# Kernel tuning notes

Hardware: AMD Instinct MI355X
Metric: run time of the kernel (lower is better)

Reference implementation:

```python
import jax, jax.numpy as jnp
import numpy as np

B, N, F_IN, HID, OUT, NHEADS = 16, 1024, 64, 64, 64, 4
TAXI = 512        # get_Parameter('taxi_size') from the original repo (node split point)
ALPHA = 0.2       # LeakyReLU negative slope


def setup_inputs() -> dict:
    key = jax.random.key(0)
    ks = jax.random.split(key, 8)
    x = jax.random.normal(ks[0], (B, N, F_IN), dtype=jnp.float32)
    # multiplicative binary mask (mostly ones so softmax rows are well-conditioned)
    mask = (jax.random.uniform(ks[1], (N, N)) > 0.1).astype(jnp.float32)
    s_in = 1.0 / np.sqrt(F_IN)
    s_cat = 1.0 / np.sqrt(NHEADS * HID)
    W1 = jax.random.normal(ks[2], (NHEADS, F_IN, HID), jnp.float32) * s_in
    W2 = jax.random.normal(ks[3], (NHEADS, F_IN, HID), jnp.float32) * s_in
    a = jax.random.normal(ks[4], (NHEADS, 2 * HID), jnp.float32) * 0.1
    W1o = jax.random.normal(ks[5], (NHEADS * HID, OUT), jnp.float32) * s_cat
    W2o = jax.random.normal(ks[6], (NHEADS * HID, OUT), jnp.float32) * s_cat
    ao = jax.random.normal(ks[7], (2 * OUT,), jnp.float32) * 0.1
    return dict(x=x, mask=mask, W1=W1, W2=W2, a=a, W1o=W1o, W2o=W2o, ao=ao)


def _gat_layer(x, mask, W1, W2, a, out_dim):
    # x: [B,N,F]; W1,W2: [F,out_dim]; a: [2*out_dim]
    # node-group-split linear projection (taxi nodes via W1, rest via W2)
    h = jnp.concatenate([x[:, :TAXI] @ W1, x[:, TAXI:] @ W2], axis=1)  # [B,N,O]
    A1 = h @ a[:out_dim]                 # [B,N]
    A2 = h @ a[out_dim:]                 # [B,N]
    sim = A1[:, :, None] + A2[:, None, :]  # [B,N,N] additive scores
    e = jax.nn.leaky_relu(sim, ALPHA)
    e = mask[None, :, :] * e             # multiplicative mask (as in source)
    attn = jax.nn.softmax(e, axis=-1)    # [B,N,N]  (dropout omitted: eval mode)
    h_prime = jnp.einsum('bnm,bmo->bno', attn, h)
    return jax.nn.elu(h_prime), attn


def reference(x, mask, W1, W2, a, W1o, W2o, ao):
    # input dropout omitted (eval mode)
    heads = [_gat_layer(x, mask, W1[i], W2[i], a[i], HID)[0] for i in range(NHEADS)]
    xc = jnp.concatenate(heads, axis=-1)          # [B,N,NHEADS*HID]
    out, attn = _gat_layer(xc, mask, W1o, W2o, ao, OUT)
    return out, attn
```

## Files before the change

### kernel.cpp

```cpp
#include <hip/hip_runtime.h>
#include <hip/hip_bf16.h>

#define B_      16
#define N_      1024
#define ALPHA_  0.2f
#define LOG2E_  1.4426950408889634f

typedef __attribute__((ext_vector_type(8)))  __bf16 bf16x8;
typedef __attribute__((ext_vector_type(4)))  float  floatx4;
typedef __attribute__((ext_vector_type(16))) float  floatx16;

__device__ __forceinline__ float eluf(float u) { return u > 0.f ? u : __expf(u) - 1.f; }

__device__ __forceinline__ float exp2fast(float x) {
#if __has_builtin(__builtin_amdgcn_exp2f)
    return __builtin_amdgcn_exp2f(x);
#else
    return exp2f(x);
#endif
}

__device__ __forceinline__ floatx4 mfma_bf16(bf16x8 a, bf16x8 b, floatx4 c) {
    return __builtin_amdgcn_mfma_f32_16x16x32_bf16(a, b, c, 0, 0, 0);
}
__device__ __forceinline__ floatx16 mfma32_bf16(bf16x8 a, bf16x8 b, floatx16 c) {
    return __builtin_amdgcn_mfma_f32_32x32x16_bf16(a, b, c, 0, 0, 0);
}

__global__ __launch_bounds__(256) void proj1_kernel(
    const float* __restrict__ x, const float* __restrict__ W1,
    const float* __restrict__ W2, const float* __restrict__ av,
    const float* __restrict__ maskG, unsigned* __restrict__ bitsOut,
    __bf16* __restrict__ h1t, float* __restrict__ A1, float* __restrict__ A2)
{
    const int tile = blockIdx.x, b = blockIdx.y, head = blockIdx.z;
    const int n0 = tile * 64;
    const float* W  = ((n0 < 512) ? W1 : W2) + head * 64 * 64;
    const float* ah = av + head * 128;

    __shared__ __align__(16) __bf16 xs[64][72];
    __shared__ __align__(16) __bf16 Wt[64][72];
    __shared__ __align__(16) float as_[128];

    const int tid = threadIdx.x;
    if (tid < 128) as_[tid] = ah[tid];
#pragma unroll
    for (int i = 0; i < 4; ++i) {
        int idx = i * 256 + tid;
        int r = idx >> 4, c = (idx & 15) * 4;
        float4 v = *(const float4*)(x + ((size_t)(b * N_ + n0 + r)) * 64 + c);
        xs[r][c+0] = (__bf16)v.x; xs[r][c+1] = (__bf16)v.y;
        xs[r][c+2] = (__bf16)v.z; xs[r][c+3] = (__bf16)v.w;
        float4 wv = *(const float4*)(W + (size_t)r * 64 + c);
        Wt[c+0][r] = (__bf16)wv.x; Wt[c+1][r] = (__bf16)wv.y;
        Wt[c+2][r] = (__bf16)wv.z; Wt[c+3][r] = (__bf16)wv.w;
    }

    {
        const int bid = blockIdx.x + 16 * (blockIdx.y + 16 * blockIdx.z);
        if (tid < 32) {
            const float* src = maskG + ((size_t)(bid * 32 + tid)) * 32;
            unsigned v = 0;
#pragma unroll
            for (int j = 0; j < 8; ++j) {
                float4 f = *(const float4*)(src + j * 4);
                v |= ((unsigned)(f.x != 0.f)) << (j * 4 + 0);
                v |= ((unsigned)(f.y != 0.f)) << (j * 4 + 1);
                v |= ((unsigned)(f.z != 0.f)) << (j * 4 + 2);
                v |= ((unsigned)(f.w != 0.f)) << (j * 4 + 3);
            }
            bitsOut[bid * 32 + tid] = v;
        }
    }
    __syncthreads();

    const int w = tid >> 6, L = tid & 63, quad = L >> 4, lo = L & 15;
    floatx4 acc[4] = {{0,0,0,0},{0,0,0,0},{0,0,0,0},{0,0,0,0}};
#pragma unroll
    for (int kc = 0; kc < 2; ++kc) {
        bf16x8 af = *(bf16x8*)&xs[16 * w + lo][kc * 32 + quad * 8];
#pragma unroll
        for (int t = 0; t < 4; ++t) {
            bf16x8 bv = *(bf16x8*)&Wt[16 * t + lo][kc * 32 + quad * 8];
            acc[t] = mfma_bf16(af, bv, acc[t]);
        }
    }

    float p1[4] = {0, 0, 0, 0}, p2[4] = {0, 0, 0, 0};
#pragma unroll
    for (int t = 0; t < 4; ++t) {
        float a1w = as_[16 * t + lo], a2w = as_[64 + 16 * t + lo];
#pragma unroll
        for (int i = 0; i < 4; ++i) { p1[i] += acc[t][i] * a1w; p2[i] += acc[t][i] * a2w; }
    }
#pragma unroll
    for (int s = 1; s < 16; s <<= 1)
#pragma unroll
        for (int i = 0; i < 4; ++i) {
            p1[i] += __shfl_xor(p1[i], s);
            p2[i] += __shfl_xor(p2[i], s);
        }
    const int bh = head * B_ + b;
    if (lo == 0) {
#pragma unroll
        for (int i = 0; i < 4; ++i) {
            int n = 16 * w + quad * 4 + i;
            A1[bh * N_ + n0 + n] = p1[i] * LOG2E_;
            A2[bh * N_ + n0 + n] = p2[i] * LOG2E_;
        }
    }

    __syncthreads();
#pragma unroll
    for (int t = 0; t < 4; ++t)
#pragma unroll
        for (int i = 0; i < 4; ++i)
            xs[16 * w + quad * 4 + i][16 * t + lo] = (__bf16)acc[t][i];
    __syncthreads();
    const int d = tid & 63, ch = tid >> 6;
    bf16x8 v0, v1;
#pragma unroll
    for (int j = 0; j < 8; ++j) v0[j] = xs[ch * 16 + j][d];
#pragma unroll
    for (int j = 0; j < 8; ++j) v1[j] = xs[ch * 16 + 8 + j][d];
    bf16x8* dst = (bf16x8*)(h1t + ((size_t)bh * 64 + d) * N_ + n0 + ch * 16);
    dst[0] = v0; dst[1] = v1;
}

__global__ __launch_bounds__(256) void attn1_kernel(
    const float* __restrict__ A1g, const float* __restrict__ A2g,
    const __bf16* __restrict__ Htg, const unsigned* __restrict__ bitsG,
    __bf16* __restrict__ xc_out)
{
    const int b = blockIdx.x, head = blockIdx.y, tile = blockIdx.z;
    const int n0 = tile * 128;
    const int bh = head * B_ + b;
    const float* A2 = A2g + (size_t)bh * N_;
    const __bf16* Hglob = Htg + (size_t)bh * 64 * N_;

    __shared__ __align__(16) __bf16 frag[2][4][2][64][8];
    __shared__ __align__(16) __bf16 ts[128][72];
    __shared__ __align__(16) float A2s[N_];
    __shared__ __align__(16) unsigned bitsS[32 * 128];
    __shared__ float invzS[128];

    const int tid = threadIdx.x;
    *(float4*)&A2s[tid * 4] = *(const float4*)(A2 + tid * 4);
    {
        const int row = tid >> 1, w0 = (tid & 1) * 16;
        uint4 u0 = *(const uint4*)(bitsG + n0 * 32 + tid * 16);
        uint4 u1 = *(const uint4*)(bitsG + n0 * 32 + tid * 16 + 4);
        uint4 u2 = *(const uint4*)(bitsG + n0 * 32 + tid * 16 + 8);
        uint4 u3 = *(const uint4*)(bitsG + n0 * 32 + tid * 16 + 12);
        bitsS[(w0+ 0)*128+row] = u0.x; bitsS[(w0+ 1)*128+row] = u0.y;
        bitsS[(w0+ 2)*128+row] = u0.z; bitsS[(w0+ 3)*128+row] = u0.w;
        bitsS[(w0+ 4)*128+row] = u1.x; bitsS[(w0+ 5)*128+row] = u1.y;
        bitsS[(w0+ 6)*128+row] = u1.z; bitsS[(w0+ 7)*128+row] = u1.w;
        bitsS[(w0+ 8)*128+row] = u2.x; bitsS[(w0+ 9)*128+row] = u2.y;
        bitsS[(w0+10)*128+row] = u2.z; bitsS[(w0+11)*128+row] = u2.w;
        bitsS[(w0+12)*128+row] = u3.x; bitsS[(w0+13)*128+row] = u3.y;
        bitsS[(w0+14)*128+row] = u3.z; bitsS[(w0+15)*128+row] = u3.w;
    }

    const int sd = tid >> 2, sq = tid & 3;
    const __bf16* hrow = Hglob + (size_t)sd * N_ + sq * 16;
    const int L = tid & 63, rg = tid >> 6, hi = L >> 5, lq = L & 31;
    const int rloc = rg * 32 + lq;
    const float a1r = A1g[(size_t)bh * N_ + n0 + rloc];

    bf16x8 h0 = *(const bf16x8*)(hrow);
    bf16x8 h1 = *(const bf16x8*)(hrow + 8);
    *(bf16x8*)&frag[0][sq][sd >> 5][(sd & 31)][0]      = h0;
    *(bf16x8*)&frag[0][sq][sd >> 5][(sd & 31) + 32][0] = h1;
    __syncthreads();

    floatx16 acc0 = {0,0,0,0,0,0,0,0,0,0,0,0,0,0,0,0};
    floatx16 acc1 = {0,0,0,0,0,0,0,0,0,0,0,0,0,0,0,0};
    float zacc = 0.f;

    for (int mt = 0; mt < 16; ++mt) {
        const int cur = mt & 1;
        if (mt < 15) {
            h0 = *(const bf16x8*)(hrow + (mt + 1) * 64);
            h1 = *(const bf16x8*)(hrow + (mt + 1) * 64 + 8);
        }
#pragma unroll
        for (int ks = 0; ks < 4; ++ks) {
            const int mbase = mt * 64 + ks * 16 + hi * 8;
            const unsigned wb = bitsS[(mbase >> 5) * 128 + rloc] >> (mbase & 31);
            float4 av  = *(const float4*)&A2s[mbase];
            float4 av2 = *(const float4*)&A2s[mbase + 4];
            float a2v[8] = {av.x, av.y, av.z, av.w, av2.x, av2.y, av2.z, av2.w};
            float o[8];
#pragma unroll
            for (int j = 0; j < 8; ++j) {
                float s = a1r + a2v[j];
                float lr = fmaxf(s, ALPHA_ * s);
                int bm = (int)(wb << (31 - j)) >> 31;
                lr = __int_as_float(__float_as_int(lr) & bm);
                float t = exp2fast(lr);
                zacc += t; o[j] = t;
            }
            bf16x8 af = {(__bf16)o[0], (__bf16)o[1], (__bf16)o[2], (__bf16)o[3],
                         (__bf16)o[4], (__bf16)o[5], (__bf16)o[6], (__bf16)o[7]};
            bf16x8 bv0 = *(bf16x8*)&frag[cur][ks][0][L][0];
            bf16x8 bv1 = *(bf16x8*)&frag[cur][ks][1][L][0];
            acc0 = mfma32_bf16(af, bv0, acc0);
            acc1 = mfma32_bf16(af, bv1, acc1);
        }
        if (mt < 15) {
            *(bf16x8*)&frag[cur ^ 1][sq][sd >> 5][(sd & 31)][0]      = h0;
            *(bf16x8*)&frag[cur ^ 1][sq][sd >> 5][(sd & 31) + 32][0] = h1;
            __syncthreads();
        }
    }

    zacc += __shfl_xor(zacc, 32);
    if (hi == 0) invzS[rloc] = 1.f / zacc;
    __syncthreads();

    float iz[16];
#pragma unroll
    for (int r = 0; r < 16; ++r)
        iz[r] = invzS[rg * 32 + (r & 3) + 8 * (r >> 2) + 4 * hi];

#pragma unroll
    for (int r = 0; r < 16; ++r) {
        const int row = rg * 32 + (r & 3) + 8 * (r >> 2) + 4 * hi;
        ts[row][lq]      = (__bf16)eluf(acc0[r] * iz[r]);
        ts[row][32 + lq] = (__bf16)eluf(acc1[r] * iz[r]);
    }
    __syncthreads();
#pragma unroll
    for (int i = 0; i < 4; ++i) {
        int cid = i * 256 + tid;
        int row = cid >> 3, c8 = (cid & 7) * 8;
        bf16x8 v = *(bf16x8*)&ts[row][c8];
        *(bf16x8*)(xc_out + ((size_t)(b * N_ + n0 + row)) * 256 + head * 64 + c8) = v;
    }
}

__global__ __launch_bounds__(256) void attn2_kernel(
    const float* __restrict__ A1g, const float* __restrict__ A2g,
    const __bf16* __restrict__ Htg, const unsigned* __restrict__ bitsG,
    float* __restrict__ out_f, float* __restrict__ attn_f)
{
    const int b = blockIdx.x, tile = blockIdx.z;
    const int n0 = tile * 32;
    const float* A2 = A2g + (size_t)b * N_;
    const __bf16* Hglob = Htg + (size_t)b * 64 * N_;

    __shared__ __align__(16) __bf16 ts2[2][32][72];
    __shared__ __align__(16) __bf16 Ht2[2][64][72];
    __shared__ __align__(16) float A2s[N_];
    __shared__ __align__(16) unsigned bitsS[1024];
    __shared__ float invz[32];

    const int tid = threadIdx.x;
    *(float4*)&A2s[tid * 4] = *(const float4*)(A2 + tid * 4);
    {
        uint4 u = *(const uint4*)(bitsG + n0 * 32 + tid * 4);
        const int row = tid >> 3, wb0 = (tid & 7) * 4;
        bitsS[(wb0+0)*32+row] = u.x; bitsS[(wb0+1)*32+row] = u.y;
        bitsS[(wb0+2)*32+row] = u.z; bitsS[(wb0+3)*32+row] = u.w;
    }

    const int r2 = tid >> 3, q2 = tid & 7;
    const float a1r = A1g[(size_t)b * N_ + n0 + r2];
    const int dr = tid >> 2, dq = tid & 3;
    const int w = tid >> 6, L = tid & 63, quad = L >> 4, lo = L & 15;
    const __bf16* hrow = Hglob + (size_t)dr * N_ + dq * 16;

    floatx4 acc2[2] = {{0,0,0,0},{0,0,0,0}};
    float zacc = 0.f;
    bf16x8 tr[16];

    __syncthreads();

    auto scores = [&](int mt) -> bf16x8 {
        const int mb = mt * 64 + q2 * 8;
        const unsigned wb = bitsS[(mt * 2 + (q2 >> 2)) * 32 + r2] >> ((q2 & 3) * 8);
        float4 alo = *(const float4*)&A2s[mb];
        float4 ahi = *(const float4*)&A2s[mb + 4];
        float a2v[8] = {alo.x, alo.y, alo.z, alo.w, ahi.x, ahi.y, ahi.z, ahi.w};
        float o[8];
#pragma unroll
        for (int j = 0; j < 8; ++j) {
            float s = a1r + a2v[j];
            float lr = fmaxf(s, ALPHA_ * s);
            int bm = (int)(wb << (31 - j)) >> 31;
            lr = __int_as_float(__float_as_int(lr) & bm);
            float t = exp2fast(lr);
            zacc += t; o[j] = t;
        }
        bf16x8 pk = {(__bf16)o[0], (__bf16)o[1], (__bf16)o[2], (__bf16)o[3],
                     (__bf16)o[4], (__bf16)o[5], (__bf16)o[6], (__bf16)o[7]};
        return pk;
    };

    {
        bf16x8 h0 = *(const bf16x8*)(hrow);
        bf16x8 h1 = *(const bf16x8*)(hrow + 8);
        bf16x8 pk = scores(0);
        tr[0] = pk;
        *(bf16x8*)&ts2[0][r2][q2 * 8]      = pk;
        *(bf16x8*)&Ht2[0][dr][dq * 16]     = h0;
        *(bf16x8*)&Ht2[0][dr][dq * 16 + 8] = h1;
    }
    __syncthreads();

#pragma unroll
    for (int mt = 0; mt < 16; ++mt) {
        const int cur = mt & 1;
        bf16x8 h0, h1, pk;
        if (mt < 15) {
            h0 = *(const bf16x8*)(hrow + (mt + 1) * 64);
            h1 = *(const bf16x8*)(hrow + (mt + 1) * 64 + 8);
            pk = scores(mt + 1);
            tr[mt + 1] = pk;
        }
#pragma unroll
        for (int c = 0; c < 2; ++c)
#pragma unroll
            for (int rt = 0; rt < 2; ++rt) {
                bf16x8 af = *(bf16x8*)&ts2[cur][16 * rt + lo][c * 32 + quad * 8];
                bf16x8 bv = *(bf16x8*)&Ht2[cur][16 * w + lo][c * 32 + quad * 8];
                acc2[rt] = mfma_bf16(af, bv, acc2[rt]);
            }
        if (mt < 15) {
            *(bf16x8*)&ts2[cur ^ 1][r2][q2 * 8]      = pk;
            *(bf16x8*)&Ht2[cur ^ 1][dr][dq * 16]     = h0;
            *(bf16x8*)&Ht2[cur ^ 1][dr][dq * 16 + 8] = h1;
            __syncthreads();
        }
    }

    zacc += __shfl_xor(zacc, 1);
    zacc += __shfl_xor(zacc, 2);
    zacc += __shfl_xor(zacc, 4);
    if (q2 == 0) invz[r2] = 1.f / zacc;
    __syncthreads();

#pragma unroll
    for (int rt = 0; rt < 2; ++rt)
#pragma unroll
        for (int i = 0; i < 4; ++i) {
            const int n = 16 * rt + quad * 4 + i;
            out_f[((size_t)(b * N_ + n0 + n)) * 64 + 16 * w + lo] =
                eluf(acc2[rt][i] * invz[n]);
        }

    const float iz = invz[r2];
    float* arow = attn_f + ((size_t)(b * N_ + n0 + r2)) * N_ + q2 * 8;
#pragma unroll
    for (int mt = 0; mt < 16; ++mt) {
        bf16x8 t8 = tr[mt];
        float4 f0 = make_float4((float)t8[0] * iz, (float)t8[1] * iz,
                                (float)t8[2] * iz, (float)t8[3] * iz);
        float4 f1 = make_float4((float)t8[4] * iz, (float)t8[5] * iz,
                                (float)t8[6] * iz, (float)t8[7] * iz);
        *(float4*)(arow + mt * 64)     = f0;
        *(float4*)(arow + mt * 64 + 4) = f1;
    }
}

__global__ __launch_bounds__(256) void proj2_kernel(
    const __bf16* __restrict__ xcb, const float* __restrict__ W1o,
    const float* __restrict__ W2o, const float* __restrict__ ao,
    __bf16* __restrict__ h2t, float* __restrict__ A1o, float* __restrict__ A2o)
{
    const int tile = blockIdx.x, b = blockIdx.y;
    const int n0 = tile * 64;
    const float* W = (n0 < 512) ? W1o : W2o;

    __shared__ __align__(16) __bf16 xs[64][264];
    __shared__ __align__(16) __bf16 Wt[64][264];
    __shared__ __align__(16) float as_[128];

    const int tid = threadIdx.x;
    if (tid < 128) as_[tid] = ao[tid];

#pragma unroll
    for (int i = 0; i < 8; ++i) {
        int idx = i * 256 + tid;
        int row = idx >> 5, c = (idx & 31) * 8;
        *(bf16x8*)&xs[row][c] =
            *(const bf16x8*)(xcb + ((size_t)(b * N_ + n0 + row)) * 256 + c);
    }
#pragma unroll
    for (int i = 0; i < 16; ++i) {
        int idx = i * 256 + tid;
        int k = idx >> 4, n4 = (idx & 15) * 4;
        float4 wv = *(const float4*)(W + (size_t)k * 64 + n4);
        Wt[n4 + 0][k] = (__bf16)wv.x;
        Wt[n4 + 1][k] = (__bf16)wv.y;
        Wt[n4 + 2][k] = (__bf16)wv.z;
        Wt[n4 + 3][k] = (__bf16)wv.w;
    }
    __syncthreads();

    const int w = tid >> 6, L = tid & 63, quad = L >> 4, lo = L & 15;
    floatx4 acc[4] = {{0,0,0,0},{0,0,0,0},{0,0,0,0},{0,0,0,0}};
#pragma unroll
    for (int kc = 0; kc < 8; ++kc) {
        bf16x8 af = *(bf16x8*)&xs[16 * w + lo][kc * 32 + quad * 8];
#pragma unroll
        for (int t = 0; t < 4; ++t) {
            bf16x8 bv = *(bf16x8*)&Wt[16 * t + lo][kc * 32 + quad * 8];
            acc[t] = mfma_bf16(af, bv, acc[t]);
        }
    }

    float p1[4] = {0, 0, 0, 0}, p2[4] = {0, 0, 0, 0};
#pragma unroll
    for (int t = 0; t < 4; ++t) {
        float a1w = as_[16 * t + lo], a2w = as_[64 + 16 * t + lo];
#pragma unroll
        for (int i = 0; i < 4; ++i) { p1[i] += acc[t][i] * a1w; p2[i] += acc[t][i] * a2w; }
    }
#pragma unroll
    for (int s = 1; s < 16; s <<= 1)
#pragma unroll
        for (int i = 0; i < 4; ++i) {
            p1[i] += __shfl_xor(p1[i], s);
            p2[i] += __shfl_xor(p2[i], s);
        }
    if (lo == 0) {
#pragma unroll
        for (int i = 0; i < 4; ++i) {
            int n = 16 * w + quad * 4 + i;
            A1o[b * N_ + n0 + n] = p1[i] * LOG2E_;
            A2o[b * N_ + n0 + n] = p2[i] * LOG2E_;
        }
    }

    __syncthreads();
#pragma unroll
    for (int t = 0; t < 4; ++t)
#pragma unroll
        for (int i = 0; i < 4; ++i)
            xs[16 * w + quad * 4 + i][16 * t + lo] = (__bf16)acc[t][i];
    __syncthreads();
    const int d = tid & 63, ch = tid >> 6;
    bf16x8 v0, v1;
#pragma unroll
    for (int j = 0; j < 8; ++j) v0[j] = xs[ch * 16 + j][d];
#pragma unroll
    for (int j = 0; j < 8; ++j) v1[j] = xs[ch * 16 + 8 + j][d];
    bf16x8* dst = (bf16x8*)(h2t + ((size_t)b * 64 + d) * N_ + n0 + ch * 16);
    dst[0] = v0; dst[1] = v1;
}

extern "C" void kernel_launch(void* const* d_in, const int* in_sizes, int n_in,
                              void* d_out, int out_size, void* d_ws, size_t ws_size,
                              hipStream_t stream)
{
    const float* x    = (const float*)d_in[0];
    const float* mask = (const float*)d_in[1];
    const float* W1   = (const float*)d_in[2];
    const float* W2   = (const float*)d_in[3];
    const float* a    = (const float*)d_in[4];
    const float* W1o  = (const float*)d_in[5];
    const float* W2o  = (const float*)d_in[6];
    const float* ao   = (const float*)d_in[7];

    float* out      = (float*)d_out;
    float* attn_out = out + (size_t)B_ * N_ * 64;

    float*    ws    = (float*)d_ws;
    float*    A1    = ws;
    float*    A2    = A1 + 65536;
    float*    A1o   = A2 + 65536;
    float*    A2o   = A1o + 16384;
    __bf16*   h1t   = (__bf16*)(A2o + 16384);
    __bf16*   h2t   = h1t + 4194304;
    __bf16*   xcb   = h2t + 1048576;
    unsigned* bitsG = (unsigned*)(xcb + 4194304);

    proj1_kernel<<<dim3(16, 16, 4), 256, 0, stream>>>(x, W1, W2, a, mask, bitsG,
                                                      h1t, A1, A2);
    attn1_kernel<<<dim3(16, 4, 8), 256, 0, stream>>>(A1, A2, h1t, bitsG, xcb);
    proj2_kernel<<<dim3(16, 16, 1), 256, 0, stream>>>(xcb, W1o, W2o, ao, h2t, A1o, A2o);
    attn2_kernel<<<dim3(16, 1, 32), 256, 0, stream>>>(A1o, A2o, h2t, bitsG, out, attn_out);
}
```

Measured before the change: 150.0 us.

## Merge heads into one proj1 block and alias attn1 shared buffers

proj1 now processes all four heads in one block, with one wave per head. The x tile is loaded once instead of four times, and the grid shrinks from 1024 to 256 blocks. Each wave now does 16 MFMAs per k-chunk, and mask bit packing is redistributed to 128 threads per block. attn1 aliases its frag and ts shared buffers into one pool and adds a launch bound of 4 blocks per CU to raise occupancy, which risks register spills.

```diff
diff --git a/kernel.cpp b/kernel.cpp
--- a/kernel.cpp
+++ b/kernel.cpp
@@ -33,17 +33,17 @@
     const float* __restrict__ maskG, unsigned* __restrict__ bitsOut,
     __bf16* __restrict__ h1t, float* __restrict__ A1, float* __restrict__ A2)
 {
-    const int tile = blockIdx.x, b = blockIdx.y, head = blockIdx.z;
+    const int tile = blockIdx.x, b = blockIdx.y;
     const int n0 = tile * 64;
-    const float* W  = ((n0 < 512) ? W1 : W2) + head * 64 * 64;
-    const float* ah = av + head * 128;
+    const float* Wbase = (n0 < 512) ? W1 : W2;
 
     __shared__ __align__(16) __bf16 xs[64][72];
-    __shared__ __align__(16) __bf16 Wt[64][72];
-    __shared__ __align__(16) float as_[128];
+    __shared__ __align__(16) __bf16 Wth[4][64][72];
+    __shared__ __align__(16) float as_[512];
 
     const int tid = threadIdx.x;
-    if (tid < 128) as_[tid] = ah[tid];
+    *(float2*)&as_[tid * 2] = *(const float2*)(av + tid * 2);
+
 #pragma unroll
     for (int i = 0; i < 4; ++i) {
         int idx = i * 256 + tid;
@@ -51,15 +51,21 @@
         float4 v = *(const float4*)(x + ((size_t)(b * N_ + n0 + r)) * 64 + c);
         xs[r][c+0] = (__bf16)v.x; xs[r][c+1] = (__bf16)v.y;
         xs[r][c+2] = (__bf16)v.z; xs[r][c+3] = (__bf16)v.w;
-        float4 wv = *(const float4*)(W + (size_t)r * 64 + c);
-        Wt[c+0][r] = (__bf16)wv.x; Wt[c+1][r] = (__bf16)wv.y;
-        Wt[c+2][r] = (__bf16)wv.z; Wt[c+3][r] = (__bf16)wv.w;
+    }
+#pragma unroll
+    for (int i = 0; i < 16; ++i) {
+        int idx = i * 256 + tid;
+        int hd = idx >> 10, e = idx & 1023;
+        int r = e >> 4, c = (e & 15) * 4;
+        float4 wv = *(const float4*)(Wbase + hd * 4096 + (size_t)r * 64 + c);
+        Wth[hd][c+0][r] = (__bf16)wv.x; Wth[hd][c+1][r] = (__bf16)wv.y;
+        Wth[hd][c+2][r] = (__bf16)wv.z; Wth[hd][c+3][r] = (__bf16)wv.w;
     }
 
     {
-        const int bid = blockIdx.x + 16 * (blockIdx.y + 16 * blockIdx.z);
-        if (tid < 32) {
-            const float* src = maskG + ((size_t)(bid * 32 + tid)) * 32;
+        const int bid = blockIdx.x + 16 * blockIdx.y;
+        if (tid < 128) {
+            const float* src = maskG + ((size_t)(bid * 128 + tid)) * 32;
             unsigned v = 0;
 #pragma unroll
             for (int j = 0; j < 8; ++j) {
@@ -69,65 +75,80 @@
                 v |= ((unsigned)(f.z != 0.f)) << (j * 4 + 2);
                 v |= ((unsigned)(f.w != 0.f)) << (j * 4 + 3);
             }
-            bitsOut[bid * 32 + tid] = v;
+            bitsOut[bid * 128 + tid] = v;
         }
     }
     __syncthreads();
 
     const int w = tid >> 6, L = tid & 63, quad = L >> 4, lo = L & 15;
-    floatx4 acc[4] = {{0,0,0,0},{0,0,0,0},{0,0,0,0},{0,0,0,0}};
-#pragma unroll
-    for (int kc = 0; kc < 2; ++kc) {
-        bf16x8 af = *(bf16x8*)&xs[16 * w + lo][kc * 32 + quad * 8];
+    floatx4 acc[4][4];
+#pragma unroll
+    for (int m = 0; m < 4; ++m)
+#pragma unroll
+        for (int t = 0; t < 4; ++t) acc[m][t] = floatx4{0, 0, 0, 0};
+
+#pragma unroll
+    for (int kc = 0; kc < 2; ++kc)
+#pragma unroll
+        for (int m = 0; m < 4; ++m) {
+            bf16x8 af = *(bf16x8*)&xs[16 * m + lo][kc * 32 + quad * 8];
+#pragma unroll
+            for (int t = 0; t < 4; ++t) {
+                bf16x8 bv = *(bf16x8*)&Wth[w][16 * t + lo][kc * 32 + quad * 8];
+                acc[m][t] = mfma_bf16(af, bv, acc[m][t]);
+            }
+        }
+
+    const int bh = w * B_ + b;
+#pragma unroll
+    for (int m = 0; m < 4; ++m) {
+        float p1[4] = {0, 0, 0, 0}, p2[4] = {0, 0, 0, 0};
 #pragma unroll
         for (int t = 0; t < 4; ++t) {
-            bf16x8 bv = *(bf16x8*)&Wt[16 * t + lo][kc * 32 + quad * 8];
-            acc[t] = mfma_bf16(af, bv, acc[t]);
-        }
-    }
-
-    float p1[4] = {0, 0, 0, 0}, p2[4] = {0, 0, 0, 0};
-#pragma unroll
-    for (int t = 0; t < 4; ++t) {
-        float a1w = as_[16 * t + lo], a2w = as_[64 + 16 * t + lo];
-#pragma unroll
-        for (int i = 0; i < 4; ++i) { p1[i] += acc[t][i] * a1w; p2[i] += acc[t][i] * a2w; }
-    }
-#pragma unroll
-    for (int s = 1; s < 16; s <<= 1)
-#pragma unroll
-        for (int i = 0; i < 4; ++i) {
-            p1[i] += __shfl_xor(p1[i], s);
-            p2[i] += __shfl_xor(p2[i], s);
-        }
-    const int bh = head * B_ + b;
-    if (lo == 0) {
-#pragma unroll
-        for (int i = 0; i < 4; ++i) {
-            int n = 16 * w + quad * 4 + i;
-            A1[bh * N_ + n0 + n] = p1[i] * LOG2E_;
-            A2[bh * N_ + n0 + n] = p2[i] * LOG2E_;
-        }
-    }
-
-    __syncthreads();
-#pragma unroll
-    for (int t = 0; t < 4; ++t)
-#pragma unroll
-        for (int i = 0; i < 4; ++i)
-            xs[16 * w + quad * 4 + i][16 * t + lo] = (__bf16)acc[t][i];
-    __syncthreads();
-    const int d = tid & 63, ch = tid >> 6;
-    bf16x8 v0, v1;
-#pragma unroll
-    for (int j = 0; j < 8; ++j) v0[j] = xs[ch * 16 + j][d];
-#pragma unroll
-    for (int j = 0; j < 8; ++j) v1[j] = xs[ch * 16 + 8 + j][d];
-    bf16x8* dst = (bf16x8*)(h1t + ((size_t)bh * 64 + d) * N_ + n0 + ch * 16);
-    dst[0] = v0; dst[1] = v1;
-}
-
-__global__ __launch_bounds__(256) void attn1_kernel(
+            float a1w = as_[w * 128 + 16 * t + lo], a2w = as_[w * 128 + 64 + 16 * t + lo];
+#pragma unroll
+            for (int i = 0; i < 4; ++i) { p1[i] += acc[m][t][i] * a1w; p2[i] += acc[m][t][i] * a2w; }
+        }
+#pragma unroll
+        for (int s = 1; s < 16; s <<= 1)
+#pragma unroll
+            for (int i = 0; i < 4; ++i) {
+                p1[i] += __shfl_xor(p1[i], s);
+                p2[i] += __shfl_xor(p2[i], s);
+            }
+        if (lo == 0) {
+#pragma unroll
+            for (int i = 0; i < 4; ++i) {
+                int n = 16 * m + quad * 4 + i;
+                A1[bh * N_ + n0 + n] = p1[i] * LOG2E_;
+                A2[bh * N_ + n0 + n] = p2[i] * LOG2E_;
+            }
+        }
+    }
+
+    __syncthreads();
+#pragma unroll
+    for (int m = 0; m < 4; ++m)
+#pragma unroll
+        for (int t = 0; t < 4; ++t)
+#pragma unroll
+            for (int i = 0; i < 4; ++i)
+                Wth[w][16 * m + quad * 4 + i][16 * t + lo] = (__bf16)acc[m][t][i];
+    __syncthreads();
+    const int d = L;
+#pragma unroll
+    for (int ch = 0; ch < 4; ++ch) {
+        bf16x8 v0, v1;
+#pragma unroll
+        for (int j = 0; j < 8; ++j) v0[j] = Wth[w][ch * 16 + j][d];
+#pragma unroll
+        for (int j = 0; j < 8; ++j) v1[j] = Wth[w][ch * 16 + 8 + j][d];
+        bf16x8* dst = (bf16x8*)(h1t + ((size_t)bh * 64 + d) * N_ + n0 + ch * 16);
+        dst[0] = v0; dst[1] = v1;
+    }
+}
+
+__global__ __launch_bounds__(256, 4) void attn1_kernel(
     const float* __restrict__ A1g, const float* __restrict__ A2g,
     const __bf16* __restrict__ Htg, const unsigned* __restrict__ bitsG,
     __bf16* __restrict__ xc_out)
@@ -138,8 +159,9 @@
     const float* A2 = A2g + (size_t)bh * N_;
     const __bf16* Hglob = Htg + (size_t)bh * 64 * N_;
 
-    __shared__ __align__(16) __bf16 frag[2][4][2][64][8];
-    __shared__ __align__(16) __bf16 ts[128][72];
+    __shared__ __align__(16) char poolc[128 * 72 * 2];
+    __bf16 (*frag)[4][2][64][8] = (__bf16(*)[4][2][64][8])poolc;
+    __bf16 (*ts)[72]            = (__bf16(*)[72])poolc;
     __shared__ __align__(16) float A2s[N_];
     __shared__ __align__(16) unsigned bitsS[32 * 128];
     __shared__ float invzS[128];
@@ -477,8 +499,8 @@
     __bf16*   xcb   = h2t + 1048576;
     unsigned* bitsG = (unsigned*)(xcb + 4194304);
 
-    proj1_kernel<<<dim3(16, 16, 4), 256, 0, stream>>>(x, W1, W2, a, mask, bitsG,
-                                                      h1t, A1, A2);
+    proj1_kernel<<<dim3(16, 16), 256, 0, stream>>>(x, W1, W2, a, mask, bitsG,
+                                                   h1t, A1, A2);
     attn1_kernel<<<dim3(16, 4, 8), 256, 0, stream>>>(A1, A2, h1t, bitsG, xcb);
     proj2_kernel<<<dim3(16, 16, 1), 256, 0, stream>>>(xcb, W1o, W2o, ao, h2t, A1o, A2o);
     attn2_kernel<<<dim3(16, 1, 32), 256, 0, stream>>>(A1o, A2o, h2t, bitsG, out, attn_out);
```

Result: slower. 154.3 us (+2.9%).

## Load MFMA B-operands directly from global memory instead of staging through LDS

Applied to the files above, without the earlier changes.

In both attention kernels, the shared-memory double buffers for the transposed H tile (frag and Ht2) are removed. Each lane now loads its own MFMA B fragment straight from global or L2 as bf16x8 vectors. In attn1 this also drops the per-iteration __syncthreads and the LDS round trip. The trade-off is redundant global loads across the four warps, which all read the same H rows, and no software prefetch ahead of the MFMAs, so load latency may be exposed.

```diff
diff --git a/kernel.cpp b/kernel.cpp
--- a/kernel.cpp
+++ b/kernel.cpp
@@ -138,7 +138,6 @@
     const float* A2 = A2g + (size_t)bh * N_;
     const __bf16* Hglob = Htg + (size_t)bh * 64 * N_;
 
-    __shared__ __align__(16) __bf16 frag[2][4][2][64][8];
     __shared__ __align__(16) __bf16 ts[128][72];
     __shared__ __align__(16) float A2s[N_];
     __shared__ __align__(16) unsigned bitsS[32 * 128];
@@ -162,16 +161,13 @@
         bitsS[(w0+14)*128+row] = u3.z; bitsS[(w0+15)*128+row] = u3.w;
     }
 
-    const int sd = tid >> 2, sq = tid & 3;
-    const __bf16* hrow = Hglob + (size_t)sd * N_ + sq * 16;
     const int L = tid & 63, rg = tid >> 6, hi = L >> 5, lq = L & 31;
     const int rloc = rg * 32 + lq;
     const float a1r = A1g[(size_t)bh * N_ + n0 + rloc];
 
-    bf16x8 h0 = *(const bf16x8*)(hrow);
-    bf16x8 h1 = *(const bf16x8*)(hrow + 8);
-    *(bf16x8*)&frag[0][sq][sd >> 5][(sd & 31)][0]      = h0;
-    *(bf16x8*)&frag[0][sq][sd >> 5][(sd & 31) + 32][0] = h1;
+    const __bf16* hb0 = Hglob + (size_t)lq * N_;
+    const __bf16* hb1 = Hglob + (size_t)(lq + 32) * N_;
+
     __syncthreads();
 
     floatx16 acc0 = {0,0,0,0,0,0,0,0,0,0,0,0,0,0,0,0};
@@ -179,10 +175,12 @@
     float zacc = 0.f;
 
     for (int mt = 0; mt < 16; ++mt) {
-        const int cur = mt & 1;
-        if (mt < 15) {
-            h0 = *(const bf16x8*)(hrow + (mt + 1) * 64);
-            h1 = *(const bf16x8*)(hrow + (mt + 1) * 64 + 8);
+        bf16x8 bv0[4], bv1[4];
+#pragma unroll
+        for (int ks = 0; ks < 4; ++ks) {
+            const int mo = mt * 64 + ks * 16 + hi * 8;
+            bv0[ks] = *(const bf16x8*)(hb0 + mo);
+            bv1[ks] = *(const bf16x8*)(hb1 + mo);
         }
 #pragma unroll
         for (int ks = 0; ks < 4; ++ks) {
@@ -203,15 +201,8 @@
             }
             bf16x8 af = {(__bf16)o[0], (__bf16)o[1], (__bf16)o[2], (__bf16)o[3],
                          (__bf16)o[4], (__bf16)o[5], (__bf16)o[6], (__bf16)o[7]};
-            bf16x8 bv0 = *(bf16x8*)&frag[cur][ks][0][L][0];
-            bf16x8 bv1 = *(bf16x8*)&frag[cur][ks][1][L][0];
-            acc0 = mfma32_bf16(af, bv0, acc0);
-            acc1 = mfma32_bf16(af, bv1, acc1);
-        }
-        if (mt < 15) {
-            *(bf16x8*)&frag[cur ^ 1][sq][sd >> 5][(sd & 31)][0]      = h0;
-            *(bf16x8*)&frag[cur ^ 1][sq][sd >> 5][(sd & 31) + 32][0] = h1;
-            __syncthreads();
+            acc0 = mfma32_bf16(af, bv0[ks], acc0);
+            acc1 = mfma32_bf16(af, bv1[ks], acc1);
         }
     }
 
@@ -251,7 +242,6 @@
     const __bf16* Hglob = Htg + (size_t)b * 64 * N_;
 
     __shared__ __align__(16) __bf16 ts2[2][32][72];
-    __shared__ __align__(16) __bf16 Ht2[2][64][72];
     __shared__ __align__(16) float A2s[N_];
     __shared__ __align__(16) unsigned bitsS[1024];
     __shared__ float invz[32];
@@ -267,9 +257,8 @@
 
     const int r2 = tid >> 3, q2 = tid & 7;
     const float a1r = A1g[(size_t)b * N_ + n0 + r2];
-    const int dr = tid >> 2, dq = tid & 3;
     const int w = tid >> 6, L = tid & 63, quad = L >> 4, lo = L & 15;
-    const __bf16* hrow = Hglob + (size_t)dr * N_ + dq * 16;
+    const __bf16* hrow2 = Hglob + (size_t)(16 * w + lo) * N_;
 
     floatx4 acc2[2] = {{0,0,0,0},{0,0,0,0}};
     float zacc = 0.f;
@@ -299,38 +288,33 @@
     };
 
     {
-        bf16x8 h0 = *(const bf16x8*)(hrow);
-        bf16x8 h1 = *(const bf16x8*)(hrow + 8);
         bf16x8 pk = scores(0);
         tr[0] = pk;
-        *(bf16x8*)&ts2[0][r2][q2 * 8]      = pk;
-        *(bf16x8*)&Ht2[0][dr][dq * 16]     = h0;
-        *(bf16x8*)&Ht2[0][dr][dq * 16 + 8] = h1;
+        *(bf16x8*)&ts2[0][r2][q2 * 8] = pk;
     }
     __syncthreads();
 
 #pragma unroll
     for (int mt = 0; mt < 16; ++mt) {
         const int cur = mt & 1;
-        bf16x8 h0, h1, pk;
+        bf16x8 pk;
         if (mt < 15) {
-            h0 = *(const bf16x8*)(hrow + (mt + 1) * 64);
-            h1 = *(const bf16x8*)(hrow + (mt + 1) * 64 + 8);
             pk = scores(mt + 1);
             tr[mt + 1] = pk;
         }
+        bf16x8 bvc[2];
+#pragma unroll
+        for (int c = 0; c < 2; ++c)
+            bvc[c] = *(const bf16x8*)(hrow2 + mt * 64 + c * 32 + quad * 8);
 #pragma unroll
         for (int c = 0; c < 2; ++c)
 #pragma unroll
             for (int rt = 0; rt < 2; ++rt) {
                 bf16x8 af = *(bf16x8*)&ts2[cur][16 * rt + lo][c * 32 + quad * 8];
-                bf16x8 bv = *(bf16x8*)&Ht2[cur][16 * w + lo][c * 32 + quad * 8];
-                acc2[rt] = mfma_bf16(af, bv, acc2[rt]);
+                acc2[rt] = mfma_bf16(af, bvc[c], acc2[rt]);
             }
         if (mt < 15) {
-            *(bf16x8*)&ts2[cur ^ 1][r2][q2 * 8]      = pk;
-            *(bf16x8*)&Ht2[cur ^ 1][dr][dq * 16]     = h0;
-            *(bf16x8*)&Ht2[cur ^ 1][dr][dq * 16 + 8] = h1;
+            *(bf16x8*)&ts2[cur ^ 1][r2][q2 * 8] = pk;
             __syncthreads();
         }
     }
```

Measured after the change: 163.0 us. 8.7% more time.
